# Kernel tuning notes

Hardware: AMD Instinct MI355X
Metric: run time of the kernel (lower is better)

The kernel has to match this reference:

```python
import jax, jax.numpy as jnp
import numpy as np

B, T, D, H, L = 256, 512, 32, 128, 32


def gru_cell(x, h, Wih, Whh, bih, bhh):
    # PyTorch GRU cell: gates ordered (r, z, n)
    gi = x @ Wih.T + bih
    gh = h @ Whh.T + bhh
    ir, iz, inn = jnp.split(gi, 3, axis=-1)
    hr, hz, hn = jnp.split(gh, 3, axis=-1)
    r = jax.nn.sigmoid(ir + hr)
    z = jax.nn.sigmoid(iz + hz)
    n = jnp.tanh(inn + r * hn)
    return (1.0 - z) * n + z * h


def run_dir(x, lengths, Wih, Whh, bih, bhh):
    # Unidirectional GRU over padded batch; masked updates emulate packed sequences:
    # carry at the end equals the hidden state at each sequence's last valid step.
    Bb, Tt, _ = x.shape
    xT = jnp.swapaxes(x, 0, 1)                                   # [T,B,Din]
    mask = (jnp.arange(Tt)[:, None] < lengths[None, :])[:, :, None]  # [T,B,1]
    h0 = jnp.zeros((Bb, Whh.shape[1]), x.dtype)

    def step(h, inp):
        x_t, m = inp
        h_new = gru_cell(x_t, h, Wih, Whh, bih, bhh)
        h = jnp.where(m, h_new, h)
        return h, jnp.where(m, h_new, jnp.zeros_like(h_new))

    h_last, out = jax.lax.scan(step, h0, (xT, mask))
    return jnp.swapaxes(out, 0, 1), h_last


def reverse_seq(x, lengths):
    # Reverse each sequence within its own valid length (positions >= length are junk,
    # callers mask them out).
    Tt = x.shape[1]
    idx = jnp.clip(lengths[:, None] - 1 - jnp.arange(Tt)[None, :], 0)
    return jnp.take_along_axis(x, idx[:, :, None], axis=1)


def vrae_forward(x, eps, enc_Wih0, enc_Whh0, enc_bih0, enc_bhh0,
                 enc_Wih12, enc_Whh12, enc_bih12, enc_bhh12,
                 dec_Wih0, dec_Whh0, dec_bih0, dec_bhh0,
                 dec_Wih1, dec_Whh1, dec_bih1, dec_bhh1,
                 W_mean, b_mean, W_logvar, b_logvar,
                 W_z2h, b_z2h, W_out, b_out, lengths):
    Bb, Tt, _ = x.shape
    valid = (jnp.arange(Tt)[None, :] < lengths[:, None])[:, :, None].astype(x.dtype)

    # --- 3-layer bidirectional encoder (packed-sequence semantics) ---
    seq = x
    for l in range(3):
        if l == 0:
            pf = (enc_Wih0[0], enc_Whh0[0], enc_bih0[0], enc_bhh0[0])
            pb = (enc_Wih0[1], enc_Whh0[1], enc_bih0[1], enc_bhh0[1])
        else:
            pf = (enc_Wih12[l-1, 0], enc_Whh12[l-1, 0], enc_bih12[l-1, 0], enc_bhh12[l-1, 0])
            pb = (enc_Wih12[l-1, 1], enc_Whh12[l-1, 1], enc_bih12[l-1, 1], enc_bhh12[l-1, 1])
        out_f, h_f = run_dir(seq, lengths, *pf)
        out_b_rev, h_b = run_dir(reverse_seq(seq, lengths), lengths, *pb)
        out_b = reverse_seq(out_b_rev, lengths) * valid
        seq = jnp.concatenate([out_f, out_b], axis=-1)

    # hidden[-2] = last-layer forward final, hidden[-1] = last-layer backward final
    hcat = jnp.concatenate([h_f, h_b], axis=-1)                  # [B, 2H]
    mean = hcat @ W_mean.T + b_mean
    logvar = hcat @ W_logvar.T + b_logvar
    z = mean + jnp.exp(0.5 * logvar) * eps

    h_init = jnp.tanh(z @ W_z2h.T + b_z2h)                       # repeated over layers

    def dec_step(carry, _):
        d_in, h1, h2 = carry
        h1n = gru_cell(d_in, h1, dec_Wih0, dec_Whh0, dec_bih0, dec_bhh0)
        h2n = gru_cell(h1n, h2, dec_Wih1, dec_Whh1, dec_bih1, dec_bhh1)
        pred = h2n @ W_out.T + b_out
        return (pred, h1n, h2n), pred

    init = (jnp.zeros((Bb, x.shape[2]), x.dtype), h_init, h_init)
    _, preds = jax.lax.scan(dec_step, init, None, length=Tt)     # [T,B,D]
    reconstruction = jnp.swapaxes(preds, 0, 1)                   # [B,T,D]
    return reconstruction, mean, logvar


def setup_inputs() -> dict:
    key = jax.random.key(0)
    ks = jax.random.split(key, 32)
    s = 0.1
    inp = {}
    inp["x"] = jax.random.normal(ks[0], (B, T, D), jnp.float32)
    lengths = jnp.sort(jax.random.randint(ks[1], (B,), 1, T + 1))[::-1]
    inp["lengths"] = lengths.at[0].set(T).astype(jnp.int32)      # sorted desc, max == T
    inp["eps"] = jax.random.normal(ks[2], (B, L), jnp.float32)
    # encoder layer 0 (input D), stacked over directions [fwd, bwd]
    inp["enc_Wih0"] = jax.random.normal(ks[3], (2, 3 * H, D)) * s
    inp["enc_Whh0"] = jax.random.normal(ks[4], (2, 3 * H, H)) * s
    inp["enc_bih0"] = jax.random.normal(ks[5], (2, 3 * H)) * s
    inp["enc_bhh0"] = jax.random.normal(ks[6], (2, 3 * H)) * s
    # encoder layers 1..2 (input 2H), [layer, dir, ...]
    inp["enc_Wih12"] = jax.random.normal(ks[7], (2, 2, 3 * H, 2 * H)) * s
    inp["enc_Whh12"] = jax.random.normal(ks[8], (2, 2, 3 * H, H)) * s
    inp["enc_bih12"] = jax.random.normal(ks[9], (2, 2, 3 * H)) * s
    inp["enc_bhh12"] = jax.random.normal(ks[10], (2, 2, 3 * H)) * s
    # decoder layer 0 (input D) and layer 1 (input H)
    inp["dec_Wih0"] = jax.random.normal(ks[11], (3 * H, D)) * s
    inp["dec_Whh0"] = jax.random.normal(ks[12], (3 * H, H)) * s
    inp["dec_bih0"] = jax.random.normal(ks[13], (3 * H,)) * s
    inp["dec_bhh0"] = jax.random.normal(ks[14], (3 * H,)) * s
    inp["dec_Wih1"] = jax.random.normal(ks[15], (3 * H, H)) * s
    inp["dec_Whh1"] = jax.random.normal(ks[16], (3 * H, H)) * s
    inp["dec_bih1"] = jax.random.normal(ks[17], (3 * H,)) * s
    inp["dec_bhh1"] = jax.random.normal(ks[18], (3 * H,)) * s
    # linears
    inp["W_mean"] = jax.random.normal(ks[19], (L, 2 * H)) * s
    inp["b_mean"] = jax.random.normal(ks[20], (L,)) * s
    inp["W_logvar"] = jax.random.normal(ks[21], (L, 2 * H)) * s
    inp["b_logvar"] = jax.random.normal(ks[22], (L,)) * s
    inp["W_z2h"] = jax.random.normal(ks[23], (H, L)) * s
    inp["b_z2h"] = jax.random.normal(ks[24], (H,)) * s
    inp["W_out"] = jax.random.normal(ks[25], (D, H)) * s
    inp["b_out"] = jax.random.normal(ks[26], (D,)) * s
    return inp


def reference(x, lengths, eps, enc_Wih0, enc_Whh0, enc_bih0, enc_bhh0,
              enc_Wih12, enc_Whh12, enc_bih12, enc_bhh12,
              dec_Wih0, dec_Whh0, dec_bih0, dec_bhh0,
              dec_Wih1, dec_Whh1, dec_bih1, dec_bhh1,
              W_mean, b_mean, W_logvar, b_logvar,
              W_z2h, b_z2h, W_out, b_out):
    return vrae_forward(x, eps, enc_Wih0, enc_Whh0, enc_bih0, enc_bhh0,
                        enc_Wih12, enc_Whh12, enc_bih12, enc_bhh12,
                        dec_Wih0, dec_Whh0, dec_bih0, dec_bhh0,
                        dec_Wih1, dec_Whh1, dec_bih1, dec_bhh1,
                        W_mean, b_mean, W_logvar, b_logvar,
                        W_z2h, b_z2h, W_out, b_out, lengths)
```

## Files before the change

kernel.cpp:

```cpp
#include <hip/hip_runtime.h>
#include <hip/hip_bf16.h>


typedef __bf16 bf16;
typedef __bf16 bf16x8 __attribute__((ext_vector_type(8)));
typedef float f32x4 __attribute__((ext_vector_type(4)));

#define MFMA(a,b,c) __builtin_amdgcn_mfma_f32_16x16x32_bf16((a),(b),(c),0,0,0)

__device__ __forceinline__ float sigm_(float x){ return 1.f/(1.f+__expf(-x)); }
__device__ __forceinline__ float tanh_(float x){
  x = fminf(15.f, fmaxf(-15.f, x));
  float e = __expf(2.f*x);
  return (e-1.f)/(e+1.f);
}
__device__ __forceinline__ float fin_(float v){ return (v - v == 0.0f) ? v : 0.0f; }

struct PrepJobs {
  const float* src[9];
  bf16* hi[9];
  bf16* lo[9];
  int n[9];
};

__global__ void prep_w(PrepJobs J){
  const int stride = gridDim.x*blockDim.x;
  const int t0 = blockIdx.x*blockDim.x + threadIdx.x;
  for (int j=0;j<9;++j){
    const float* __restrict__ s = J.src[j];
    bf16* __restrict__ h = J.hi[j];
    bf16* __restrict__ l = J.lo[j];
    const int n = J.n[j];
    for (int i=t0;i<n;i+=stride){
      float v = fin_(s[i]);
      bf16 hh = (bf16)v;
      h[i] = hh;
      l[i] = (bf16)(v - (float)hh);
    }
  }
}

template<int KIN, bool F32IN>
__global__ __launch_bounds__(512,2)
void enc_rec(const void* __restrict__ seqIn_,
             bf16* __restrict__ seqOut,
             const bf16* __restrict__ WihHi_, const bf16* __restrict__ WihLo_,
             const bf16* __restrict__ WhhHi_, const bf16* __restrict__ WhhLo_,
             const float* __restrict__ bih_, const float* __restrict__ bhh_,
             const int* __restrict__ lengths,
             float* __restrict__ hFo, float* __restrict__ hBo)
{
  constexpr int NKS  = KIN/32;
  constexpr int XSTR = F32IN ? 40 : 264;
  constexpr int XPL  = 16*XSTR;
  constexpr int XSLOT= (F32IN?2:1)*XPL;
  const int tid = threadIdx.x;
  const int wave = tid>>6;
  const int lh   = tid&15;
  const int quad = (tid>>4)&3;
  const int dir  = blockIdx.x>>4;
  const int b0   = (blockIdx.x&15)*16;

  const bf16* __restrict__ WihHi = WihHi_ + (size_t)dir*384*KIN;
  const bf16* __restrict__ WihLo = WihLo_ + (size_t)dir*384*KIN;
  const bf16* __restrict__ WhhHi = WhhHi_ + (size_t)dir*384*128;
  const bf16* __restrict__ WhhLo = WhhLo_ + (size_t)dir*384*128;
  const float* __restrict__ bih = bih_ + dir*384;
  const float* __restrict__ bhh = bhh_ + dir*384;

  __shared__ bf16 hHi[16*136], hLo[16*136];
  __shared__ bf16 xb[4*XSLOT];

  const int jc = wave*16 + lh;
  const int cR = jc, cZ = 128+jc, cN = 256+jc;

  bf16x8 wRH[4],wRL[4],wZH[4],wZL[4],wNH[4],wNL[4];
#pragma unroll
  for (int ks=0;ks<4;++ks){
    const int o = ks*32 + quad*8;
    wRH[ks]=*(const bf16x8*)(WhhHi+(size_t)cR*128+o); wRL[ks]=*(const bf16x8*)(WhhLo+(size_t)cR*128+o);
    wZH[ks]=*(const bf16x8*)(WhhHi+(size_t)cZ*128+o); wZL[ks]=*(const bf16x8*)(WhhLo+(size_t)cZ*128+o);
    wNH[ks]=*(const bf16x8*)(WhhHi+(size_t)cN*128+o); wNL[ks]=*(const bf16x8*)(WhhLo+(size_t)cN*128+o);
  }
  const float bR  = bih[cR]+bhh[cR];
  const float bZc = bih[cZ]+bhh[cZ];
  const float bNi = bih[cN];
  const float bNh = bhh[cN];

  int lenRow[4];
#pragma unroll
  for (int r=0;r<4;++r) lenRow[r] = lengths[b0 + quad*4 + r];
  const int lenA = lengths[b0+lh];
  const int Tmax = lengths[b0];
  const int TT   = (Tmax+3)&~3;

  const int wrow = (tid>>4)&15;
  const int wcol = (tid&15)*8;
  const int lenW = lengths[b0 + wrow];
  const int srow = tid>>5;
  const int scol = tid&31;
  const int lenS = lengths[b0 + srow];

  for (int i=tid;i<16*136;i+=512){ hHi[i]=(bf16)0.f; hLo[i]=(bf16)0.f; }

  auto stage = [&](int slot, int sabs){
    int tb = dir ? (lenS-1-sabs) : sabs;
    tb = tb<0 ? 0 : (tb>511 ? 511 : tb);
    if constexpr (F32IN){
      float v = ((const float*)seqIn_)[((size_t)(b0+srow)*512+tb)*32 + scol];
      bf16 hh=(bf16)v;
      xb[slot*XSLOT + srow*XSTR + scol] = hh;
      xb[slot*XSLOT + XPL + srow*XSTR + scol] = (bf16)(v-(float)hh);
    } else {
      bf16x8 v = *(const bf16x8*)((const bf16*)seqIn_ + ((size_t)(b0+srow)*512+tb)*256 + scol*8);
      *(bf16x8*)&xb[slot*XSLOT + srow*XSTR + scol*8] = v;
    }
  };
#pragma unroll
  for (int s=0;s<4;++s) stage(s, 1+s);

  f32x4 accR[4], accZ[4], giN[4];
#pragma unroll
  for (int s=0;s<4;++s){
    accR[s]=(f32x4){0.f,0.f,0.f,0.f}; accZ[s]=(f32x4){0.f,0.f,0.f,0.f}; giN[s]=(f32x4){0.f,0.f,0.f,0.f};
  }

  {
    int tb0 = dir ? (lenA-1) : 0; tb0 = tb0<0?0:tb0;
#pragma unroll
    for (int ks=0;ks<NKS;++ks){
      const int o = ks*32 + quad*8;
      bf16x8 axH, axL;
      if constexpr (F32IN){
        const float* ap = (const float*)seqIn_ + ((size_t)(b0+lh)*512+tb0)*KIN + o;
#pragma unroll
        for (int e=0;e<8;++e){ float v=ap[e]; bf16 hh=(bf16)v; axH[e]=hh; axL[e]=(bf16)(v-(float)hh); }
      } else {
        axH = *(const bf16x8*)((const bf16*)seqIn_ + ((size_t)(b0+lh)*512+tb0)*KIN + o);
      }
      bf16x8 bH, bL;
      bH=*(const bf16x8*)(WihHi+(size_t)cR*KIN+o); bL=*(const bf16x8*)(WihLo+(size_t)cR*KIN+o);
      accR[3]=MFMA(axH,bH,accR[3]); if constexpr(F32IN) accR[3]=MFMA(axL,bH,accR[3]); accR[3]=MFMA(axH,bL,accR[3]);
      bH=*(const bf16x8*)(WihHi+(size_t)cZ*KIN+o); bL=*(const bf16x8*)(WihLo+(size_t)cZ*KIN+o);
      accZ[3]=MFMA(axH,bH,accZ[3]); if constexpr(F32IN) accZ[3]=MFMA(axL,bH,accZ[3]); accZ[3]=MFMA(axH,bL,accZ[3]);
      bH=*(const bf16x8*)(WihHi+(size_t)cN*KIN+o); bL=*(const bf16x8*)(WihLo+(size_t)cN*KIN+o);
      giN[3]=MFMA(axH,bH,giN[3]);  if constexpr(F32IN) giN[3]=MFMA(axL,bH,giN[3]);  giN[3]=MFMA(axH,bL,giN[3]);
    }
  }
  __syncthreads();

  for (int t4=0; t4<TT; t4+=4){
#pragma unroll
    for (int p=0;p<4;++p){
      const int t = t4 + p;
      const int s = (p+3)&3;
      if (seqOut && tid<256 && t>0 && (t-1)<lenW){
        const int tp = t-1;
        const int tb = dir ? (lenW-1-tp) : tp;
        bf16x8 v = *(const bf16x8*)&hHi[wrow*136 + wcol];
        *(bf16x8*)(seqOut + ((size_t)(b0+wrow)*512 + tb)*256 + dir*128 + wcol) = v;
      }
      f32x4 gN = {0.f,0.f,0.f,0.f};
#pragma unroll
      for (int ks=0;ks<4;++ks){
        bf16x8 aH = *(const bf16x8*)&hHi[lh*136 + ks*32 + quad*8];
        bf16x8 aL = *(const bf16x8*)&hLo[lh*136 + ks*32 + quad*8];
        accR[s]=MFMA(aH,wRH[ks],accR[s]); accR[s]=MFMA(aL,wRH[ks],accR[s]); accR[s]=MFMA(aH,wRL[ks],accR[s]);
        accZ[s]=MFMA(aH,wZH[ks],accZ[s]); accZ[s]=MFMA(aL,wZH[ks],accZ[s]); accZ[s]=MFMA(aH,wZL[ks],accZ[s]);
        gN     =MFMA(aH,wNH[ks],gN);      gN     =MFMA(aL,wNH[ks],gN);      gN     =MFMA(aH,wNL[ks],gN);
      }
      float hsel[4];
#pragma unroll
      for (int r=0;r<4;++r){
        const int m = quad*4 + r;
        float rr = sigm_(accR[s][r] + bR);
        float zz = sigm_(accZ[s][r] + bZc);
        float nn = tanh_(giN[s][r] + bNi + rr*(gN[r] + bNh));
        float hold = (float)hHi[m*136+jc] + (float)hLo[m*136+jc];
        float hnew = fin_((1.f-zz)*nn + zz*hold);
        hsel[r] = (t < lenRow[r]) ? hnew : hold;
      }
      if (p==0){
#pragma unroll
        for (int s2=0;s2<4;++s2){
          accR[s2]=(f32x4){0.f,0.f,0.f,0.f}; accZ[s2]=(f32x4){0.f,0.f,0.f,0.f}; giN[s2]=(f32x4){0.f,0.f,0.f,0.f};
        }
#pragma unroll
        for (int ks=0;ks<NKS;++ks){
          const int o = ks*32 + quad*8;
          bf16x8 axH[4], axL[F32IN?4:1];
#pragma unroll
          for (int s2=0;s2<4;++s2){
            axH[s2] = *(const bf16x8*)&xb[s2*XSLOT + lh*XSTR + o];
            if constexpr (F32IN) axL[s2] = *(const bf16x8*)&xb[s2*XSLOT + XPL + lh*XSTR + o];
          }
          bf16x8 bH, bL;
          bH=*(const bf16x8*)(WihHi+(size_t)cR*KIN+o); bL=*(const bf16x8*)(WihLo+(size_t)cR*KIN+o);
#pragma unroll
          for (int s2=0;s2<4;++s2){
            accR[s2]=MFMA(axH[s2],bH,accR[s2]);
            if constexpr(F32IN) accR[s2]=MFMA(axL[s2],bH,accR[s2]);
            accR[s2]=MFMA(axH[s2],bL,accR[s2]);
          }
          bH=*(const bf16x8*)(WihHi+(size_t)cZ*KIN+o); bL=*(const bf16x8*)(WihLo+(size_t)cZ*KIN+o);
#pragma unroll
          for (int s2=0;s2<4;++s2){
            accZ[s2]=MFMA(axH[s2],bH,accZ[s2]);
            if constexpr(F32IN) accZ[s2]=MFMA(axL[s2],bH,accZ[s2]);
            accZ[s2]=MFMA(axH[s2],bL,accZ[s2]);
          }
          bH=*(const bf16x8*)(WihHi+(size_t)cN*KIN+o); bL=*(const bf16x8*)(WihLo+(size_t)cN*KIN+o);
#pragma unroll
          for (int s2=0;s2<4;++s2){
            giN[s2]=MFMA(axH[s2],bH,giN[s2]);
            if constexpr(F32IN) giN[s2]=MFMA(axL[s2],bH,giN[s2]);
            giN[s2]=MFMA(axH[s2],bL,giN[s2]);
          }
        }
      }
      __syncthreads();
#pragma unroll
      for (int r=0;r<4;++r){
        const int m = quad*4 + r;
        bf16 hi = (bf16)hsel[r];
        hHi[m*136+jc] = hi;
        hLo[m*136+jc] = (bf16)(hsel[r]-(float)hi);
      }
      if      (p==1){ stage(0, t4+5); stage(1, t4+6); }
      else if (p==2){ stage(2, t4+7); }
      else if (p==3){ stage(3, t4+8); }
      __syncthreads();
    }
  }
  if (seqOut && tid<256 && (TT-1)<lenW){
    const int tb = dir ? (lenW-1-(TT-1)) : (TT-1);
    bf16x8 v = *(const bf16x8*)&hHi[wrow*136 + wcol];
    *(bf16x8*)(seqOut + ((size_t)(b0+wrow)*512 + tb)*256 + dir*128 + wcol) = v;
  }
  float* hout = dir ? hBo : hFo;
  if (hout && tid<256){
#pragma unroll
    for (int e=0;e<8;++e){
      const int j = wcol+e;
      hout[(size_t)(b0+wrow)*128 + j] = fin_((float)hHi[wrow*136+j] + (float)hLo[wrow*136+j]);
    }
  }
}

__global__ void latent_k(const float* __restrict__ hF, const float* __restrict__ hB,
                         const float* __restrict__ eps,
                         const float* __restrict__ Wm, const float* __restrict__ bm,
                         const float* __restrict__ Wl, const float* __restrict__ bl,
                         const float* __restrict__ Wz, const float* __restrict__ bz,
                         float* __restrict__ out_mean, float* __restrict__ out_logvar,
                         float* __restrict__ hInit)
{
  const int b = blockIdx.x, tid = threadIdx.x;
  __shared__ float hc[256];
  __shared__ float mv[64];
  __shared__ float zz[32];
  for (int k=tid;k<256;k+=64) hc[k] = fin_((k<128)? hF[(size_t)b*128+k] : hB[(size_t)b*128+k-128]);
  __syncthreads();
  {
    const int i = tid & 31;
    const float* W = (tid<32)? Wm : Wl;
    float acc = (tid<32)? bm[i] : bl[i];
    for (int k=0;k<256;++k) acc += hc[k]*W[i*256+k];
    acc = fin_(acc);
    mv[tid] = acc;
    if (tid<32) out_mean[b*32+i] = acc;
    else        out_logvar[b*32+(tid-32)] = acc;
  }
  __syncthreads();
  if (tid<32) zz[tid] = fin_(mv[tid] + __expf(0.5f*mv[32+tid]) * eps[b*32+tid]);
  __syncthreads();
  for (int j=tid;j<128;j+=64){
    float a = bz[j];
    for (int k=0;k<32;++k) a += zz[k]*Wz[j*32+k];
    hInit[(size_t)b*128 + j] = tanh_(fin_(a));
  }
}

__global__ __launch_bounds__(512,2)
void dec_rec(const float* __restrict__ hInit,
             const bf16* __restrict__ W0iH, const bf16* __restrict__ W0iL,
             const bf16* __restrict__ W0hH, const bf16* __restrict__ W0hL,
             const bf16* __restrict__ W1iH, const bf16* __restrict__ W1iL,
             const bf16* __restrict__ W1hH, const bf16* __restrict__ W1hL,
             const bf16* __restrict__ WoH,  const bf16* __restrict__ WoL,
             const float* __restrict__ bih0, const float* __restrict__ bhh0,
             const float* __restrict__ bih1, const float* __restrict__ bhh1,
             const float* __restrict__ bout,
             float* __restrict__ rec)
{
  const int tid = threadIdx.x;
  const int wave = tid>>6;
  const int lh   = tid&15;
  const int quad = (tid>>4)&3;
  const int b0 = blockIdx.x*16;
  const int jc = wave*16 + lh;
  const int cR = jc, cZ = 128+jc, cN = 256+jc;

  __shared__ bf16 h1H[16*136], h1L[16*136], h2H[16*136], h2L[16*136];
  __shared__ bf16 pH[16*40], pL[16*40];

  bf16x8 a0RH[4],a0RL[4],a0ZH[4],a0ZL[4],a0NH[4],a0NL[4];
  bf16x8 a1RH[4],a1RL[4],a1ZH[4],a1ZL[4],a1NH[4],a1NL[4];
#pragma unroll
  for (int ks=0;ks<4;++ks){
    const int o = ks*32 + quad*8;
    a0RH[ks]=*(const bf16x8*)(W0hH+(size_t)cR*128+o); a0RL[ks]=*(const bf16x8*)(W0hL+(size_t)cR*128+o);
    a0ZH[ks]=*(const bf16x8*)(W0hH+(size_t)cZ*128+o); a0ZL[ks]=*(const bf16x8*)(W0hL+(size_t)cZ*128+o);
    a0NH[ks]=*(const bf16x8*)(W0hH+(size_t)cN*128+o); a0NL[ks]=*(const bf16x8*)(W0hL+(size_t)cN*128+o);
    a1RH[ks]=*(const bf16x8*)(W1hH+(size_t)cR*128+o); a1RL[ks]=*(const bf16x8*)(W1hL+(size_t)cR*128+o);
    a1ZH[ks]=*(const bf16x8*)(W1hH+(size_t)cZ*128+o); a1ZL[ks]=*(const bf16x8*)(W1hL+(size_t)cZ*128+o);
    a1NH[ks]=*(const bf16x8*)(W1hH+(size_t)cN*128+o); a1NL[ks]=*(const bf16x8*)(W1hL+(size_t)cN*128+o);
  }
  const float b1R = bih0[cR]+bhh0[cR], b1Z = bih0[cZ]+bhh0[cZ], b1Ni = bih0[cN], b1Nh = bhh0[cN];
  const float b2R = bih1[cR]+bhh1[cR], b2Z = bih1[cZ]+bhh1[cZ], b2Ni = bih1[cN], b2Nh = bhh1[cN];
  const float bo = (wave<2) ? bout[wave*16+lh] : 0.f;

  if (tid < 256){
    const int row = (tid>>4)&15;
    const int c0  = (tid&15)*8;
#pragma unroll
    for (int e=0;e<8;++e){
      const int j = c0+e;
      float v = fin_(hInit[(size_t)(b0+row)*128 + j]);
      bf16 hi=(bf16)v, lo=(bf16)(v-(float)hi);
      h1H[row*136+j]=hi; h1L[row*136+j]=lo;
      h2H[row*136+j]=hi; h2L[row*136+j]=lo;
    }
  }
  for (int i=tid;i<16*40;i+=512){ pH[i]=(bf16)0.f; pL[i]=(bf16)0.f; }
  __syncthreads();

  for (int t=0;t<512;++t){
    f32x4 xR={0.f,0.f,0.f,0.f}, xZ={0.f,0.f,0.f,0.f}, xNi={0.f,0.f,0.f,0.f}, xNh={0.f,0.f,0.f,0.f};
    {
      bf16x8 aP0 = *(const bf16x8*)&pH[lh*40 + quad*8];
      bf16x8 aP1 = *(const bf16x8*)&pL[lh*40 + quad*8];
      const int o = quad*8;
      bf16x8 bH,bL;
      bH=*(const bf16x8*)(W0iH+(size_t)cR*32+o); bL=*(const bf16x8*)(W0iL+(size_t)cR*32+o);
      xR=MFMA(aP0,bH,xR); xR=MFMA(aP1,bH,xR); xR=MFMA(aP0,bL,xR);
      bH=*(const bf16x8*)(W0iH+(size_t)cZ*32+o); bL=*(const bf16x8*)(W0iL+(size_t)cZ*32+o);
      xZ=MFMA(aP0,bH,xZ); xZ=MFMA(aP1,bH,xZ); xZ=MFMA(aP0,bL,xZ);
      bH=*(const bf16x8*)(W0iH+(size_t)cN*32+o); bL=*(const bf16x8*)(W0iL+(size_t)cN*32+o);
      xNi=MFMA(aP0,bH,xNi); xNi=MFMA(aP1,bH,xNi); xNi=MFMA(aP0,bL,xNi);
    }
#pragma unroll
    for (int ks=0;ks<4;++ks){
      bf16x8 aH = *(const bf16x8*)&h1H[lh*136 + ks*32 + quad*8];
      bf16x8 aL = *(const bf16x8*)&h1L[lh*136 + ks*32 + quad*8];
      xR =MFMA(aH,a0RH[ks],xR);  xR =MFMA(aL,a0RH[ks],xR);  xR =MFMA(aH,a0RL[ks],xR);
      xZ =MFMA(aH,a0ZH[ks],xZ);  xZ =MFMA(aL,a0ZH[ks],xZ);  xZ =MFMA(aH,a0ZL[ks],xZ);
      xNh=MFMA(aH,a0NH[ks],xNh); xNh=MFMA(aL,a0NH[ks],xNh); xNh=MFMA(aH,a0NL[ks],xNh);
    }
    float h1n[4];
#pragma unroll
    for (int r=0;r<4;++r){
      const int m = quad*4+r;
      float rr = sigm_(xR[r] + b1R);
      float z  = sigm_(xZ[r] + b1Z);
      float nn = tanh_(xNi[r] + b1Ni + rr*(xNh[r] + b1Nh));
      float hold = (float)h1H[m*136+jc] + (float)h1L[m*136+jc];
      h1n[r] = fin_((1.f-z)*nn + z*hold);
    }
    __syncthreads();
#pragma unroll
    for (int r=0;r<4;++r){
      const int m = quad*4+r;
      bf16 hi=(bf16)h1n[r];
      h1H[m*136+jc]=hi; h1L[m*136+jc]=(bf16)(h1n[r]-(float)hi);
    }
    __syncthreads();
    xR=(f32x4){0.f,0.f,0.f,0.f}; xZ=(f32x4){0.f,0.f,0.f,0.f};
    xNi=(f32x4){0.f,0.f,0.f,0.f}; xNh=(f32x4){0.f,0.f,0.f,0.f};
#pragma unroll
    for (int ks=0;ks<4;++ks){
      const int o = ks*32 + quad*8;
      bf16x8 aH = *(const bf16x8*)&h1H[lh*136 + o];
      bf16x8 aL = *(const bf16x8*)&h1L[lh*136 + o];
      bf16x8 bH,bL;
      bH=*(const bf16x8*)(W1iH+(size_t)cR*128+o); bL=*(const bf16x8*)(W1iL+(size_t)cR*128+o);
      xR=MFMA(aH,bH,xR); xR=MFMA(aL,bH,xR); xR=MFMA(aH,bL,xR);
      bH=*(const bf16x8*)(W1iH+(size_t)cZ*128+o); bL=*(const bf16x8*)(W1iL+(size_t)cZ*128+o);
      xZ=MFMA(aH,bH,xZ); xZ=MFMA(aL,bH,xZ); xZ=MFMA(aH,bL,xZ);
      bH=*(const bf16x8*)(W1iH+(size_t)cN*128+o); bL=*(const bf16x8*)(W1iL+(size_t)cN*128+o);
      xNi=MFMA(aH,bH,xNi); xNi=MFMA(aL,bH,xNi); xNi=MFMA(aH,bL,xNi);
    }
#pragma unroll
    for (int ks=0;ks<4;++ks){
      bf16x8 aH = *(const bf16x8*)&h2H[lh*136 + ks*32 + quad*8];
      bf16x8 aL = *(const bf16x8*)&h2L[lh*136 + ks*32 + quad*8];
      xR =MFMA(aH,a1RH[ks],xR);  xR =MFMA(aL,a1RH[ks],xR);  xR =MFMA(aH,a1RL[ks],xR);
      xZ =MFMA(aH,a1ZH[ks],xZ);  xZ =MFMA(aL,a1ZH[ks],xZ);  xZ =MFMA(aH,a1ZL[ks],xZ);
      xNh=MFMA(aH,a1NH[ks],xNh); xNh=MFMA(aL,a1NH[ks],xNh); xNh=MFMA(aH,a1NL[ks],xNh);
    }
    float h2n[4];
#pragma unroll
    for (int r=0;r<4;++r){
      const int m = quad*4+r;
      float rr = sigm_(xR[r] + b2R);
      float z  = sigm_(xZ[r] + b2Z);
      float nn = tanh_(xNi[r] + b2Ni + rr*(xNh[r] + b2Nh));
      float hold = (float)h2H[m*136+jc] + (float)h2L[m*136+jc];
      h2n[r] = fin_((1.f-z)*nn + z*hold);
    }
    __syncthreads();
#pragma unroll
    for (int r=0;r<4;++r){
      const int m = quad*4+r;
      bf16 hi=(bf16)h2n[r];
      h2H[m*136+jc]=hi; h2L[m*136+jc]=(bf16)(h2n[r]-(float)hi);
    }
    __syncthreads();
    if (wave<2){
      f32x4 po={0.f,0.f,0.f,0.f};
#pragma unroll
      for (int ks=0;ks<4;++ks){
        const int o = ks*32 + quad*8;
        bf16x8 oH = *(const bf16x8*)&h2H[lh*136 + o];
        bf16x8 oL = *(const bf16x8*)&h2L[lh*136 + o];
        bf16x8 bH = *(const bf16x8*)(WoH + (size_t)(wave*16+lh)*128 + o);
        bf16x8 bL = *(const bf16x8*)(WoL + (size_t)(wave*16+lh)*128 + o);
        po=MFMA(oH,bH,po); po=MFMA(oL,bH,po); po=MFMA(oH,bL,po);
      }
#pragma unroll
      for (int r=0;r<4;++r){
        const int m = quad*4+r;
        float pv = fin_(po[r]+bo);
        rec[((size_t)(b0+m)*512 + t)*32 + wave*16+lh] = pv;
        bf16 hi=(bf16)pv;
        pH[m*40 + wave*16+lh]=hi; pL[m*40 + wave*16+lh]=(bf16)(pv-(float)hi);
      }
    }
    __syncthreads();
  }
}

extern "C" void kernel_launch(void* const* d_in, const int* in_sizes, int n_in,
                              void* d_out, int out_size, void* d_ws, size_t ws_size,
                              hipStream_t stream)
{
  const float* x       = (const float*)d_in[0];
  const int*   lengths = (const int*)d_in[1];
  const float* eps     = (const float*)d_in[2];
  const float* eWih0   = (const float*)d_in[3];
  const float* eWhh0   = (const float*)d_in[4];
  const float* ebih0   = (const float*)d_in[5];
  const float* ebhh0   = (const float*)d_in[6];
  const float* eWih12  = (const float*)d_in[7];
  const float* eWhh12  = (const float*)d_in[8];
  const float* ebih12  = (const float*)d_in[9];
  const float* ebhh12  = (const float*)d_in[10];
  const float* dWih0   = (const float*)d_in[11];
  const float* dWhh0   = (const float*)d_in[12];
  const float* dbih0   = (const float*)d_in[13];
  const float* dbhh0   = (const float*)d_in[14];
  const float* dWih1   = (const float*)d_in[15];
  const float* dWhh1   = (const float*)d_in[16];
  const float* dbih1   = (const float*)d_in[17];
  const float* dbhh1   = (const float*)d_in[18];
  const float* Wm      = (const float*)d_in[19];
  const float* bm      = (const float*)d_in[20];
  const float* Wl      = (const float*)d_in[21];
  const float* bl      = (const float*)d_in[22];
  const float* Wz      = (const float*)d_in[23];
  const float* bz      = (const float*)d_in[24];
  const float* Wo      = (const float*)d_in[25];
  const float* bo      = (const float*)d_in[26];

  char* ws = (char*)d_ws;
  bf16* P     = (bf16*)ws;
  bf16* seqA  = (bf16*)(ws + (size_t)(4<<20));
  bf16* seqB  = (bf16*)(ws + (size_t)(68<<20));
  float* hF    = (float*)seqA;
  float* hB    = hF + 256*128;
  float* hInit = hB + 256*128;

  const size_t O_eWih0  = 0;
  const size_t O_eWhh0  = 49152;
  const size_t O_eWih12 = 245760;
  const size_t O_eWhh12 = 1032192;
  const size_t O_dWih0  = 1425408;
  const size_t O_dWhh0  = 1449984;
  const size_t O_dWih1  = 1548288;
  const size_t O_dWhh1  = 1646592;
  const size_t O_Wout   = 1744896;

  float* out   = (float*)d_out;
  float* rec   = out;
  float* omean = out + (size_t)4194304;
  float* ologv = omean + 8192;

  size_t zoff = (size_t)(4<<20);
  size_t zbytes = (size_t)(128<<20);
  if (zoff + zbytes > ws_size) zbytes = (ws_size > zoff)? ws_size - zoff : 0;
  hipMemsetAsync(ws + zoff, 0, zbytes, stream);

  PrepJobs J;
  const float* srcs[9] = {eWih0, eWhh0, eWih12, eWhh12, dWih0, dWhh0, dWih1, dWhh1, Wo};
  const size_t offs[9] = {O_eWih0,O_eWhh0,O_eWih12,O_eWhh12,O_dWih0,O_dWhh0,O_dWih1,O_dWhh1,O_Wout};
  const int    ns[9]   = {24576, 98304, 393216, 196608, 12288, 49152, 49152, 49152, 4096};
  for (int j=0;j<9;++j){ J.src[j]=srcs[j]; J.hi[j]=P+offs[j]; J.lo[j]=P+offs[j]+ns[j]; J.n[j]=ns[j]; }
  prep_w<<<256, 256, 0, stream>>>(J);

  dim3 blk(512);

  enc_rec<32,true><<<32, blk, 0, stream>>>(x, seqA,
      P+O_eWih0, P+O_eWih0+24576, P+O_eWhh0, P+O_eWhh0+98304,
      ebih0, ebhh0, lengths, nullptr, nullptr);
  enc_rec<256,false><<<32, blk, 0, stream>>>(seqA, seqB,
      P+O_eWih12, P+O_eWih12+393216, P+O_eWhh12, P+O_eWhh12+196608,
      ebih12, ebhh12, lengths, nullptr, nullptr);
  enc_rec<256,false><<<32, blk, 0, stream>>>(seqB, nullptr,
      P+O_eWih12+196608, P+O_eWih12+393216+196608,
      P+O_eWhh12+98304,  P+O_eWhh12+196608+98304,
      ebih12+768, ebhh12+768, lengths, hF, hB);
  latent_k<<<256, 64, 0, stream>>>(hF, hB, eps, Wm, bm, Wl, bl, Wz, bz,
                                   omean, ologv, hInit);
  dec_rec<<<16, blk, 0, stream>>>(hInit,
      P+O_dWih0, P+O_dWih0+12288, P+O_dWhh0, P+O_dWhh0+49152,
      P+O_dWih1, P+O_dWih1+49152, P+O_dWhh1, P+O_dWhh1+49152,
      P+O_Wout,  P+O_Wout+4096,
      dbih0, dbhh0, dbih1, dbhh1, bo, rec);
}
```

Baseline: 10.25 ms.

## Precompute decoder hidden-gate MFMAs early, cut barriers, stage W1i hi in LDS

The decoder step loop is reorganised. The recurrent h@Whh products for both layers are computed at the end of the previous step, right after the output projection, so only the input-side MFMAs remain on the critical path. Each hidden state is now updated in place, which removes two __syncthreads per timestep. The high half of the layer-1 input weights is staged in a large shared-memory buffer, and the register-resident weights are pinned with empty asm so the compiler keeps them in registers. The trade-off is more LDS use, about 104KB, which could limit occupancy, and more register pressure from six live accumulators carried across steps.

New measurement: 9.803 ms. 4.4% less time.

```diff
diff --git a/kernel.cpp b/kernel.cpp
--- a/kernel.cpp
+++ b/kernel.cpp
@@ -7,6 +7,7 @@
 typedef float f32x4 __attribute__((ext_vector_type(4)));
 
 #define MFMA(a,b,c) __builtin_amdgcn_mfma_f32_16x16x32_bf16((a),(b),(c),0,0,0)
+#define Z4 (f32x4){0.f,0.f,0.f,0.f}
 
 __device__ __forceinline__ float sigm_(float x){ return 1.f/(1.f+__expf(-x)); }
 __device__ __forceinline__ float tanh_(float x){
@@ -15,6 +16,7 @@
   return (e-1.f)/(e+1.f);
 }
 __device__ __forceinline__ float fin_(float v){ return (v - v == 0.0f) ? v : 0.0f; }
+__device__ __forceinline__ void pin_(bf16x8 &v){ asm volatile("" : "+v"(v)); }
 
 struct PrepJobs {
   const float* src[9];
@@ -81,6 +83,7 @@
     wRH[ks]=*(const bf16x8*)(WhhHi+(size_t)cR*128+o); wRL[ks]=*(const bf16x8*)(WhhLo+(size_t)cR*128+o);
     wZH[ks]=*(const bf16x8*)(WhhHi+(size_t)cZ*128+o); wZL[ks]=*(const bf16x8*)(WhhLo+(size_t)cZ*128+o);
     wNH[ks]=*(const bf16x8*)(WhhHi+(size_t)cN*128+o); wNL[ks]=*(const bf16x8*)(WhhLo+(size_t)cN*128+o);
+    pin_(wRH[ks]); pin_(wRL[ks]); pin_(wZH[ks]); pin_(wZL[ks]); pin_(wNH[ks]); pin_(wNL[ks]);
   }
   const float bR  = bih[cR]+bhh[cR];
   const float bZc = bih[cZ]+bhh[cZ];
@@ -121,9 +124,7 @@
 
   f32x4 accR[4], accZ[4], giN[4];
 #pragma unroll
-  for (int s=0;s<4;++s){
-    accR[s]=(f32x4){0.f,0.f,0.f,0.f}; accZ[s]=(f32x4){0.f,0.f,0.f,0.f}; giN[s]=(f32x4){0.f,0.f,0.f,0.f};
-  }
+  for (int s=0;s<4;++s){ accR[s]=Z4; accZ[s]=Z4; giN[s]=Z4; }
 
   {
     int tb0 = dir ? (lenA-1) : 0; tb0 = tb0<0?0:tb0;
@@ -160,7 +161,7 @@
         bf16x8 v = *(const bf16x8*)&hHi[wrow*136 + wcol];
         *(bf16x8*)(seqOut + ((size_t)(b0+wrow)*512 + tb)*256 + dir*128 + wcol) = v;
       }
-      f32x4 gN = {0.f,0.f,0.f,0.f};
+      f32x4 gN = Z4;
 #pragma unroll
       for (int ks=0;ks<4;++ks){
         bf16x8 aH = *(const bf16x8*)&hHi[lh*136 + ks*32 + quad*8];
@@ -182,9 +183,7 @@
       }
       if (p==0){
 #pragma unroll
-        for (int s2=0;s2<4;++s2){
-          accR[s2]=(f32x4){0.f,0.f,0.f,0.f}; accZ[s2]=(f32x4){0.f,0.f,0.f,0.f}; giN[s2]=(f32x4){0.f,0.f,0.f,0.f};
-        }
+        for (int s2=0;s2<4;++s2){ accR[s2]=Z4; accZ[s2]=Z4; giN[s2]=Z4; }
 #pragma unroll
         for (int ks=0;ks<NKS;++ks){
           const int o = ks*32 + quad*8;
@@ -303,6 +302,7 @@
 
   __shared__ bf16 h1H[16*136], h1L[16*136], h2H[16*136], h2L[16*136];
   __shared__ bf16 pH[16*40], pL[16*40];
+  __shared__ bf16 w1iLds[384*136];
 
   bf16x8 a0RH[4],a0RL[4],a0ZH[4],a0ZL[4],a0NH[4],a0NL[4];
   bf16x8 a1RH[4],a1RL[4],a1ZH[4],a1ZL[4],a1NH[4],a1NL[4];
@@ -315,11 +315,17 @@
     a1RH[ks]=*(const bf16x8*)(W1hH+(size_t)cR*128+o); a1RL[ks]=*(const bf16x8*)(W1hL+(size_t)cR*128+o);
     a1ZH[ks]=*(const bf16x8*)(W1hH+(size_t)cZ*128+o); a1ZL[ks]=*(const bf16x8*)(W1hL+(size_t)cZ*128+o);
     a1NH[ks]=*(const bf16x8*)(W1hH+(size_t)cN*128+o); a1NL[ks]=*(const bf16x8*)(W1hL+(size_t)cN*128+o);
+    pin_(a0RH[ks]); pin_(a0RL[ks]); pin_(a0ZH[ks]); pin_(a0ZL[ks]); pin_(a0NH[ks]); pin_(a0NL[ks]);
+    pin_(a1RH[ks]); pin_(a1RL[ks]); pin_(a1ZH[ks]); pin_(a1ZL[ks]); pin_(a1NH[ks]); pin_(a1NL[ks]);
   }
   const float b1R = bih0[cR]+bhh0[cR], b1Z = bih0[cZ]+bhh0[cZ], b1Ni = bih0[cN], b1Nh = bhh0[cN];
   const float b2R = bih1[cR]+bhh1[cR], b2Z = bih1[cZ]+bhh1[cZ], b2Ni = bih1[cN], b2Nh = bhh1[cN];
   const float bo = (wave<2) ? bout[wave*16+lh] : 0.f;
 
+  for (int i=tid; i<384*16; i+=512){
+    const int rr = i>>4, k8 = (i&15)*8;
+    *(bf16x8*)&w1iLds[rr*136 + k8] = *(const bf16x8*)(W1iH + (size_t)rr*128 + k8);
+  }
   if (tid < 256){
     const int row = (tid>>4)&15;
     const int c0  = (tid&15)*8;
@@ -335,89 +341,87 @@
   for (int i=tid;i<16*40;i+=512){ pH[i]=(bf16)0.f; pL[i]=(bf16)0.f; }
   __syncthreads();
 
+  f32x4 c1R, c1Z, c1Nh, c2R, c2Z, c2Nh;
+
+  auto ghpre = [&](){
+    c1R=Z4; c1Z=Z4; c1Nh=Z4; c2R=Z4; c2Z=Z4; c2Nh=Z4;
+#pragma unroll
+    for (int ks=0;ks<4;++ks){
+      const int o = ks*32 + quad*8;
+      bf16x8 aH = *(const bf16x8*)&h1H[lh*136 + o];
+      bf16x8 aL = *(const bf16x8*)&h1L[lh*136 + o];
+      c1R =MFMA(aH,a0RH[ks],c1R);  c1R =MFMA(aL,a0RH[ks],c1R);  c1R =MFMA(aH,a0RL[ks],c1R);
+      c1Z =MFMA(aH,a0ZH[ks],c1Z);  c1Z =MFMA(aL,a0ZH[ks],c1Z);  c1Z =MFMA(aH,a0ZL[ks],c1Z);
+      c1Nh=MFMA(aH,a0NH[ks],c1Nh); c1Nh=MFMA(aL,a0NH[ks],c1Nh); c1Nh=MFMA(aH,a0NL[ks],c1Nh);
+    }
+#pragma unroll
+    for (int ks=0;ks<4;++ks){
+      const int o = ks*32 + quad*8;
+      bf16x8 aH = *(const bf16x8*)&h2H[lh*136 + o];
+      bf16x8 aL = *(const bf16x8*)&h2L[lh*136 + o];
+      c2R =MFMA(aH,a1RH[ks],c2R);  c2R =MFMA(aL,a1RH[ks],c2R);  c2R =MFMA(aH,a1RL[ks],c2R);
+      c2Z =MFMA(aH,a1ZH[ks],c2Z);  c2Z =MFMA(aL,a1ZH[ks],c2Z);  c2Z =MFMA(aH,a1ZL[ks],c2Z);
+      c2Nh=MFMA(aH,a1NH[ks],c2Nh); c2Nh=MFMA(aL,a1NH[ks],c2Nh); c2Nh=MFMA(aH,a1NL[ks],c2Nh);
+    }
+  };
+  ghpre();
+
   for (int t=0;t<512;++t){
-    f32x4 xR={0.f,0.f,0.f,0.f}, xZ={0.f,0.f,0.f,0.f}, xNi={0.f,0.f,0.f,0.f}, xNh={0.f,0.f,0.f,0.f};
     {
+      f32x4 c1Ni = Z4;
       bf16x8 aP0 = *(const bf16x8*)&pH[lh*40 + quad*8];
       bf16x8 aP1 = *(const bf16x8*)&pL[lh*40 + quad*8];
       const int o = quad*8;
       bf16x8 bH,bL;
       bH=*(const bf16x8*)(W0iH+(size_t)cR*32+o); bL=*(const bf16x8*)(W0iL+(size_t)cR*32+o);
-      xR=MFMA(aP0,bH,xR); xR=MFMA(aP1,bH,xR); xR=MFMA(aP0,bL,xR);
+      c1R=MFMA(aP0,bH,c1R); c1R=MFMA(aP1,bH,c1R); c1R=MFMA(aP0,bL,c1R);
       bH=*(const bf16x8*)(W0iH+(size_t)cZ*32+o); bL=*(const bf16x8*)(W0iL+(size_t)cZ*32+o);
-      xZ=MFMA(aP0,bH,xZ); xZ=MFMA(aP1,bH,xZ); xZ=MFMA(aP0,bL,xZ);
+      c1Z=MFMA(aP0,bH,c1Z); c1Z=MFMA(aP1,bH,c1Z); c1Z=MFMA(aP0,bL,c1Z);
       bH=*(const bf16x8*)(W0iH+(size_t)cN*32+o); bL=*(const bf16x8*)(W0iL+(size_t)cN*32+o);
-      xNi=MFMA(aP0,bH,xNi); xNi=MFMA(aP1,bH,xNi); xNi=MFMA(aP0,bL,xNi);
-    }
-#pragma unroll
-    for (int ks=0;ks<4;++ks){
-      bf16x8 aH = *(const bf16x8*)&h1H[lh*136 + ks*32 + quad*8];
-      bf16x8 aL = *(const bf16x8*)&h1L[lh*136 + ks*32 + quad*8];
-      xR =MFMA(aH,a0RH[ks],xR);  xR =MFMA(aL,a0RH[ks],xR);  xR =MFMA(aH,a0RL[ks],xR);
-      xZ =MFMA(aH,a0ZH[ks],xZ);  xZ =MFMA(aL,a0ZH[ks],xZ);  xZ =MFMA(aH,a0ZL[ks],xZ);
-      xNh=MFMA(aH,a0NH[ks],xNh); xNh=MFMA(aL,a0NH[ks],xNh); xNh=MFMA(aH,a0NL[ks],xNh);
-    }
-    float h1n[4];
-#pragma unroll
-    for (int r=0;r<4;++r){
-      const int m = quad*4+r;
-      float rr = sigm_(xR[r] + b1R);
-      float z  = sigm_(xZ[r] + b1Z);
-      float nn = tanh_(xNi[r] + b1Ni + rr*(xNh[r] + b1Nh));
-      float hold = (float)h1H[m*136+jc] + (float)h1L[m*136+jc];
-      h1n[r] = fin_((1.f-z)*nn + z*hold);
+      c1Ni=MFMA(aP0,bH,c1Ni); c1Ni=MFMA(aP1,bH,c1Ni); c1Ni=MFMA(aP0,bL,c1Ni);
+#pragma unroll
+      for (int r=0;r<4;++r){
+        const int m = quad*4+r;
+        float rr = sigm_(c1R[r] + b1R);
+        float z  = sigm_(c1Z[r] + b1Z);
+        float nn = tanh_(c1Ni[r] + b1Ni + rr*(c1Nh[r] + b1Nh));
+        float hold = (float)h1H[m*136+jc] + (float)h1L[m*136+jc];
+        float hnew = fin_((1.f-z)*nn + z*hold);
+        bf16 hi=(bf16)hnew;
+        h1H[m*136+jc]=hi; h1L[m*136+jc]=(bf16)(hnew-(float)hi);
+      }
     }
     __syncthreads();
-#pragma unroll
-    for (int r=0;r<4;++r){
-      const int m = quad*4+r;
-      bf16 hi=(bf16)h1n[r];
-      h1H[m*136+jc]=hi; h1L[m*136+jc]=(bf16)(h1n[r]-(float)hi);
-    }
-    __syncthreads();
-    xR=(f32x4){0.f,0.f,0.f,0.f}; xZ=(f32x4){0.f,0.f,0.f,0.f};
-    xNi=(f32x4){0.f,0.f,0.f,0.f}; xNh=(f32x4){0.f,0.f,0.f,0.f};
-#pragma unroll
-    for (int ks=0;ks<4;++ks){
-      const int o = ks*32 + quad*8;
-      bf16x8 aH = *(const bf16x8*)&h1H[lh*136 + o];
-      bf16x8 aL = *(const bf16x8*)&h1L[lh*136 + o];
-      bf16x8 bH,bL;
-      bH=*(const bf16x8*)(W1iH+(size_t)cR*128+o); bL=*(const bf16x8*)(W1iL+(size_t)cR*128+o);
-      xR=MFMA(aH,bH,xR); xR=MFMA(aL,bH,xR); xR=MFMA(aH,bL,xR);
-      bH=*(const bf16x8*)(W1iH+(size_t)cZ*128+o); bL=*(const bf16x8*)(W1iL+(size_t)cZ*128+o);
-      xZ=MFMA(aH,bH,xZ); xZ=MFMA(aL,bH,xZ); xZ=MFMA(aH,bL,xZ);
-      bH=*(const bf16x8*)(W1iH+(size_t)cN*128+o); bL=*(const bf16x8*)(W1iL+(size_t)cN*128+o);
-      xNi=MFMA(aH,bH,xNi); xNi=MFMA(aL,bH,xNi); xNi=MFMA(aH,bL,xNi);
-    }
-#pragma unroll
-    for (int ks=0;ks<4;++ks){
-      bf16x8 aH = *(const bf16x8*)&h2H[lh*136 + ks*32 + quad*8];
-      bf16x8 aL = *(const bf16x8*)&h2L[lh*136 + ks*32 + quad*8];
-      xR =MFMA(aH,a1RH[ks],xR);  xR =MFMA(aL,a1RH[ks],xR);  xR =MFMA(aH,a1RL[ks],xR);
-      xZ =MFMA(aH,a1ZH[ks],xZ);  xZ =MFMA(aL,a1ZH[ks],xZ);  xZ =MFMA(aH,a1ZL[ks],xZ);
-      xNh=MFMA(aH,a1NH[ks],xNh); xNh=MFMA(aL,a1NH[ks],xNh); xNh=MFMA(aH,a1NL[ks],xNh);
-    }
-    float h2n[4];
-#pragma unroll
-    for (int r=0;r<4;++r){
-      const int m = quad*4+r;
-      float rr = sigm_(xR[r] + b2R);
-      float z  = sigm_(xZ[r] + b2Z);
-      float nn = tanh_(xNi[r] + b2Ni + rr*(xNh[r] + b2Nh));
-      float hold = (float)h2H[m*136+jc] + (float)h2L[m*136+jc];
-      h2n[r] = fin_((1.f-z)*nn + z*hold);
-    }
-    __syncthreads();
-#pragma unroll
-    for (int r=0;r<4;++r){
-      const int m = quad*4+r;
-      bf16 hi=(bf16)h2n[r];
-      h2H[m*136+jc]=hi; h2L[m*136+jc]=(bf16)(h2n[r]-(float)hi);
+    {
+      f32x4 c2Ni = Z4;
+#pragma unroll
+      for (int ks=0;ks<4;++ks){
+        const int o = ks*32 + quad*8;
+        bf16x8 aH = *(const bf16x8*)&h1H[lh*136 + o];
+        bf16x8 aL = *(const bf16x8*)&h1L[lh*136 + o];
+        bf16x8 bH,bL;
+        bH=*(const bf16x8*)&w1iLds[cR*136+o]; bL=*(const bf16x8*)(W1iL+(size_t)cR*128+o);
+        c2R=MFMA(aH,bH,c2R); c2R=MFMA(aL,bH,c2R); c2R=MFMA(aH,bL,c2R);
+        bH=*(const bf16x8*)&w1iLds[cZ*136+o]; bL=*(const bf16x8*)(W1iL+(size_t)cZ*128+o);
+        c2Z=MFMA(aH,bH,c2Z); c2Z=MFMA(aL,bH,c2Z); c2Z=MFMA(aH,bL,c2Z);
+        bH=*(const bf16x8*)&w1iLds[cN*136+o]; bL=*(const bf16x8*)(W1iL+(size_t)cN*128+o);
+        c2Ni=MFMA(aH,bH,c2Ni); c2Ni=MFMA(aL,bH,c2Ni); c2Ni=MFMA(aH,bL,c2Ni);
+      }
+#pragma unroll
+      for (int r=0;r<4;++r){
+        const int m = quad*4+r;
+        float rr = sigm_(c2R[r] + b2R);
+        float z  = sigm_(c2Z[r] + b2Z);
+        float nn = tanh_(c2Ni[r] + b2Ni + rr*(c2Nh[r] + b2Nh));
+        float hold = (float)h2H[m*136+jc] + (float)h2L[m*136+jc];
+        float hnew = fin_((1.f-z)*nn + z*hold);
+        bf16 hi=(bf16)hnew;
+        h2H[m*136+jc]=hi; h2L[m*136+jc]=(bf16)(hnew-(float)hi);
+      }
     }
     __syncthreads();
     if (wave<2){
-      f32x4 po={0.f,0.f,0.f,0.f};
+      f32x4 po=Z4;
 #pragma unroll
       for (int ks=0;ks<4;++ks){
         const int o = ks*32 + quad*8;
@@ -436,6 +440,7 @@
         pH[m*40 + wave*16+lh]=hi; pL[m*40 + wave*16+lh]=(bf16)(pv-(float)hi);
       }
     }
+    if (t+1 < 512) ghpre();
     __syncthreads();
   }
 }
```
